# Kernel optimization log

Measured on AMD Instinct MI355X. Metric: run time of the kernel, lower is better.

The kernel has to match this reference:

```python
import jax, jax.numpy as jnp
import numpy as np

D_MODEL = 1024
NHEAD = 16
HEAD_DIM = D_MODEL // NHEAD
FF = 4096
ALPHA = 1.4142135  # deepnorm_alpha
WIN = (127, 128)   # sliding window (left, right)
EPS = 1e-5
ROPE_BASE = 10000.0


def rmsnorm(x, g):
    ms = jnp.mean(x * x, axis=-1, keepdims=True)
    return x * jax.lax.rsqrt(ms + EPS) * g


def rope(x):
    # x: [B, T, H, D]; non-interleaved rotary over full head dim
    T, D = x.shape[1], x.shape[-1]
    half = D // 2
    inv_freq = 1.0 / (ROPE_BASE ** (jnp.arange(half, dtype=jnp.float32) * 2.0 / D))
    ang = jnp.arange(T, dtype=jnp.float32)[:, None] * inv_freq[None, :]  # [T, half]
    cos = jnp.cos(ang)[None, :, None, :]
    sin = jnp.sin(ang)[None, :, None, :]
    x1, x2 = x[..., :half], x[..., half:]
    return jnp.concatenate([x1 * cos - x2 * sin, x2 * cos + x1 * sin], axis=-1)


def setup_inputs() -> dict:
    key = jax.random.key(0)
    ks = jax.random.split(key, 8)
    d, h = D_MODEL, FF
    return {
        "x": jax.random.normal(ks[0], (2, 2048, d), jnp.float32),
        "Wqkv": jax.random.normal(ks[1], (3 * d, d), jnp.float32) * 0.02,
        "Wout": jax.random.normal(ks[2], (d, d), jnp.float32) * 0.02,
        "bout": jnp.zeros((d,), jnp.float32),
        "W1": jax.random.normal(ks[3], (2 * h, d), jnp.float32) * 0.02,
        "W2": jax.random.normal(ks[4], (d, h), jnp.float32) * 0.02,
        "g1": jnp.ones((d,), jnp.float32),
        "g2": jnp.ones((d,), jnp.float32),
    }


def reference(x, Wqkv, Wout, bout, W1, W2, g1, g2):
    B, T, d = x.shape
    # --- self attention with RoPE + sliding window band mask ---
    qkv = (x @ Wqkv.T).reshape(B, T, 3, NHEAD, HEAD_DIM)
    q, k, v = qkv[:, :, 0], qkv[:, :, 1], qkv[:, :, 2]  # [B,T,H,Dh]
    q = rope(q)
    k = rope(k)
    q = jnp.swapaxes(q, 1, 2)  # [B,H,T,Dh]
    k = jnp.swapaxes(k, 1, 2)
    v = jnp.swapaxes(v, 1, 2)
    scale = 1.0 / np.sqrt(HEAD_DIM)
    scores = jnp.einsum('bhqd,bhkd->bhqk', q, k) * scale
    idx = jnp.arange(T)
    rel = idx[None, :] - idx[:, None]  # j - i
    band = (rel >= -WIN[0]) & (rel <= WIN[1])  # [T,T] allowed positions
    scores = jnp.where(band[None, None], scores, -jnp.inf)
    attn = jax.nn.softmax(scores, axis=-1)
    o = jnp.einsum('bhqk,bhkd->bhqd', attn, v)
    o = jnp.swapaxes(o, 1, 2).reshape(B, T, d)
    a = o @ Wout.T + bout
    # --- deepnorm residual 1 + RMSNorm ---
    x1 = a + ALPHA * x
    x2 = rmsnorm(x1, g1)
    # --- SwiGLU MLP: y, gate = fc1(x).chunk(2); y*gate*sigmoid(gate) ---
    yg = x2 @ W1.T
    y, gate = jnp.split(yg, 2, axis=-1)
    y = y * gate * jax.nn.sigmoid(gate)
    y = y @ W2.T
    # --- deepnorm residual 2 + RMSNorm ---
    x3 = y + ALPHA * x2
    return rmsnorm(x3, g2)
```

## Files before the change

### kernel.cpp

```cpp
#include <hip/hip_runtime.h>

#define T_SEQ   2048
#define NHEADS  16
#define DHEAD   64
#define DMODEL  1024
#define ALPHA_C 1.4142135f
#define EPS_C   1e-5f

typedef __attribute__((ext_vector_type(8))) short bf16x8;
typedef __attribute__((ext_vector_type(4))) short bf16x4;
typedef __attribute__((ext_vector_type(4))) float floatx4;

__device__ __forceinline__ float bf2f(unsigned short u) {
  union { unsigned int i; float f; } v;
  v.i = ((unsigned int)u) << 16;
  return v.f;
}
__device__ __forceinline__ unsigned short f2bf(float f) {
  union { float f; unsigned int i; } v;
  v.f = f;
  unsigned int u = v.i;
  u += 0x7FFF + ((u >> 16) & 1);
  return (unsigned short)(u >> 16);
}

__device__ __forceinline__ void gload_lds16(const void* g, void* l) {
  __builtin_amdgcn_global_load_lds(
      (const __attribute__((address_space(1))) void*)g,
      (__attribute__((address_space(3))) void*)l, 16, 0, 0);
}

__global__ void convert_all(const float* __restrict__ Wqkv,
                            const float* __restrict__ Wout,
                            const float* __restrict__ W1,
                            const float* __restrict__ W2,
                            const float* __restrict__ x,
                            unsigned short* __restrict__ ws,
                            float* __restrict__ cosT,
                            float* __restrict__ sinT)
{
  if (blockIdx.x >= 10240) {
    int gid = (blockIdx.x - 10240) * 256 + threadIdx.x;
    int t = gid >> 5, i = gid & 31;
    float fr = powf(10000.f, -(float)i * (1.f / 32.f));
    float sn, cs;
    sincosf((float)t * fr, &sn, &cs);
    cosT[gid] = cs;
    sinT[gid] = sn;
    return;
  }
  size_t i = ((size_t)blockIdx.x * 256 + threadIdx.x) * 8;
  const float* src;
  size_t off;
  if      (i <  3145728) { src = Wqkv; off = i; }
  else if (i <  4194304) { src = Wout; off = i -  3145728; }
  else if (i < 12582912) { src = W1;   off = i -  4194304; }
  else if (i < 16777216) { src = W2;   off = i - 12582912; }
  else                   { src = x;    off = i - 16777216; }
  floatx4 a = *(const floatx4*)(src + off);
  floatx4 b = *(const floatx4*)(src + off + 4);
  bf16x8 o;
  #pragma unroll
  for (int u = 0; u < 4; u++) {
    o[u]     = (short)f2bf(a[u]);
    o[4 + u] = (short)f2bf(b[u]);
  }
  *(bf16x8*)(ws + i) = o;
}

template<int BN>
__global__ __launch_bounds__(256) void gemm_lds(
    const unsigned short* __restrict__ A,
    const unsigned short* __restrict__ W,
    unsigned short* __restrict__ C,
    const float* __restrict__ bias,
    int M, int N, int K, int lda)
{
  constexpr int WN = BN / 2;
  constexpr int NJ = WN / 16;
  __shared__ unsigned short As[128 * 32];
  __shared__ unsigned short Bs[BN * 32];

  const int tid  = threadIdx.x;
  const int lane = tid & 63;
  const int wave = tid >> 6;
  const int wm = (wave >> 1) * 64;
  const int wn = (wave & 1) * WN;
  const int mBase = blockIdx.y * 128;
  const int nBase = blockIdx.x * BN;

  const int sRow = lane >> 2;
  const int sCol = (lane & 3) * 8;

  floatx4 acc[4][NJ];
  #pragma unroll
  for (int i = 0; i < 4; i++)
    #pragma unroll
    for (int j = 0; j < NJ; j++) acc[i][j] = (floatx4){0.f, 0.f, 0.f, 0.f};

  const int mrow = lane & 15;
  const int kq   = (lane >> 4) * 8;

  for (int kb = 0; kb < K; kb += 32) {
    __syncthreads();
    #pragma unroll
    for (int j = 0; j < 2; j++) {
      int r = wave * 32 + j * 16 + sRow;
      gload_lds16(A + (size_t)(mBase + r) * lda + kb + sCol,
                  &As[wave * 1024 + j * 512 + lane * 8]);
    }
    if constexpr (BN == 128) {
      #pragma unroll
      for (int j = 0; j < 2; j++) {
        int r = wave * 32 + j * 16 + sRow;
        gload_lds16(W + (size_t)(nBase + r) * K + kb + sCol,
                    &Bs[wave * 1024 + j * 512 + lane * 8]);
      }
    } else {
      int r = wave * 16 + sRow;
      gload_lds16(W + (size_t)(nBase + r) * K + kb + sCol,
                  &Bs[wave * 512 + lane * 8]);
    }
    __syncthreads();

    bf16x8 af[4], bfr[NJ];
    #pragma unroll
    for (int i = 0; i < 4; i++)
      af[i] = *(const bf16x8*)&As[(wm + i * 16 + mrow) * 32 + kq];
    #pragma unroll
    for (int j = 0; j < NJ; j++)
      bfr[j] = *(const bf16x8*)&Bs[(wn + j * 16 + mrow) * 32 + kq];
    #pragma unroll
    for (int i = 0; i < 4; i++)
      #pragma unroll
      for (int j = 0; j < NJ; j++)
        acc[i][j] = __builtin_amdgcn_mfma_f32_16x16x32_bf16(af[i], bfr[j], acc[i][j], 0, 0, 0);
  }

  const int col0 = lane & 15;
  const int row0 = (lane >> 4) * 4;
  #pragma unroll
  for (int j = 0; j < NJ; j++) {
    const int col = nBase + wn + j * 16 + col0;
    const float badd = bias ? bias[col] : 0.f;
    #pragma unroll
    for (int i = 0; i < 4; i++) {
      #pragma unroll
      for (int r = 0; r < 4; r++) {
        const int row = mBase + wm + i * 16 + row0 + r;
        C[(size_t)row * N + col] = f2bf(acc[i][j][r] + badd);
      }
    }
  }
}

#define BAR() __builtin_amdgcn_s_barrier()
#define SCB() __builtin_amdgcn_sched_barrier(0)

#define RD_A_S(bb, mh, s)                                                 \
  _Pragma("unroll") for (int i = 0; i < 4; i++)                           \
    af[i][s] = *(const bf16x8*)&lds[(bb) + aRd +                          \
        ((mh) * 64 + i * 16 + mrow) * 64 + (kq0 ^ ((s) << 5))];

#define RD_B_S(bb, s)                                                     \
  _Pragma("unroll") for (int n = 0; n < 4; n++)                           \
    bfr[n][s] = *(const bf16x8*)&lds[(bb) + bRd +                         \
        (bRow0 + n * 16 + mrow) * 64 + (kq0 ^ ((s) << 5))];

#define MFMA8(mh, nh, s)                                                  \
  _Pragma("unroll") for (int i = 0; i < 4; i++)                           \
  _Pragma("unroll") for (int n = 0; n < 2; n++)                           \
    acc[(mh) * 4 + i][(nh) * 2 + n] =                                     \
        __builtin_amdgcn_mfma_f32_16x16x32_bf16(                          \
            af[i][s], bfr[(nh) * 2 + n][s],                               \
            acc[(mh) * 4 + i][(nh) * 2 + n], 0, 0, 0);

#define KLOOP_S4()                                                        \
  for (int t = 0; t < 16; ++t) {                                          \
    const int cur = t & 1;                                                \
    const int nxt = cur ^ 1;                                              \
    const int bb  = cur * 32768;                                          \
    const int ta  = (t + 1 < 16) ? t + 1 : 15;                            \
    const int tb  = (t + 2 < 16) ? t + 2 : 15;                            \
                                                             \
    BAR();                                                                \
    stA(nxt, 1, ta);                                                      \
    RD_A_S(bb, 0, 0); RD_B_S(bb, 0);                                      \
    SCB();                                                                \
    RD_A_S(bb, 0, 1); RD_B_S(bb, 1);                                      \
    asm volatile("s_waitcnt lgkmcnt(8)" ::: "memory");                    \
    SCB();                                                                \
    __builtin_amdgcn_s_setprio(1);                                        \
    MFMA8(0, 0, 0);                                                       \
    __builtin_amdgcn_s_setprio(0);                                        \
    asm volatile("s_waitcnt lgkmcnt(0)" ::: "memory");                    \
    SCB();                                                                \
    __builtin_amdgcn_s_setprio(1);                                        \
    MFMA8(0, 0, 1);                                                       \
    __builtin_amdgcn_s_setprio(0);                                        \
                                                             \
    BAR();                                                                \
    stB(nxt, 1, ta);                                                      \
    __builtin_amdgcn_s_setprio(1);                                        \
    MFMA8(0, 1, 0); MFMA8(0, 1, 1);                                       \
    __builtin_amdgcn_s_setprio(0);                                        \
                                                             \
    BAR();                                                                \
    stB(cur, 0, tb);                                                      \
    RD_A_S(bb, 1, 0);                                                     \
    SCB();                                                                \
    RD_A_S(bb, 1, 1);                                                     \
    asm volatile("s_waitcnt lgkmcnt(4)" ::: "memory");                    \
    SCB();                                                                \
    __builtin_amdgcn_s_setprio(1);                                        \
    MFMA8(1, 1, 0);                                                       \
    __builtin_amdgcn_s_setprio(0);                                        \
    asm volatile("s_waitcnt lgkmcnt(0)" ::: "memory");                    \
    SCB();                                                                \
    __builtin_amdgcn_s_setprio(1);                                        \
    MFMA8(1, 1, 1);                                                       \
    __builtin_amdgcn_s_setprio(0);                                        \
                                                             \
    BAR();                                                                \
    stA(cur, 0, tb);                                                      \
    __builtin_amdgcn_s_setprio(1);                                        \
    MFMA8(1, 0, 0); MFMA8(1, 0, 1);                                       \
    __builtin_amdgcn_s_setprio(0);                                        \
    asm volatile("s_waitcnt vmcnt(4)" ::: "memory");                      \
  }

__global__ __launch_bounds__(512, 2) void gemm_w1_swiglu_s4(
    const unsigned short* __restrict__ A,
    const unsigned short* __restrict__ W1,
    unsigned short* __restrict__ ys)
{
  __shared__ unsigned short lds[65536];

  const int tid  = threadIdx.x;
  const int lane = tid & 63;
  const int wid  = tid >> 6;
  const int wr   = wid >> 2;
  const int wc   = wid & 3;
  const int mrow = lane & 15;
  const int quad = lane >> 4;
  const int kq0  = (quad ^ (mrow & 7)) * 8;

  const int bid  = blockIdx.x;
  const int c8   = bid & 7;
  const int u    = bid >> 3;
  const int mBase = ((c8 >> 2) * 8 + (u >> 3)) * 256;
  const int nBase = ((c8 &  3) * 8 + (u &  7)) * 128;

  const int r0 = tid >> 3;
  const int ce = (((tid & 7) ^ (r0 & 7)) * 8);
  const size_t aoff0 = (size_t)(mBase + r0) * 1024 + ce;
  const size_t aoff1 = aoff0 + (size_t)64 * 1024;
  auto growf = [&](int br) {
    int col = nBase + (br >> 6) * 32 + (br & 31);
    return ((br >> 5) & 1) ? 4096 + col : col;
  };
  const size_t boff00 = (size_t)growf(r0)       * 1024 + ce;
  const size_t boff01 = (size_t)growf(64 + r0)  * 1024 + ce;
  const size_t boff10 = (size_t)growf(128 + r0) * 1024 + ce;
  const size_t boff11 = (size_t)growf(192 + r0) * 1024 + ce;
  const int d0 = tid * 8;

  auto stA = [&](int buf, int h, int kt) {
    const unsigned short* g = A + (size_t)kt * 64 + (h ? (size_t)128 * 1024 : 0);
    int base = buf * 32768 + h * 8192;
    gload_lds16(g + aoff0, &lds[base + d0]);
    gload_lds16(g + aoff1, &lds[base + 4096 + d0]);
  };
  auto stB = [&](int buf, int h, int kt) {
    const unsigned short* g = W1 + (size_t)kt * 64;
    int base = buf * 32768 + 16384 + h * 8192;
    gload_lds16(g + (h ? boff10 : boff00), &lds[base + d0]);
    gload_lds16(g + (h ? boff11 : boff01), &lds[base + 4096 + d0]);
  };

  floatx4 acc[8][4];
  #pragma unroll
  for (int i = 0; i < 8; i++)
    #pragma unroll
    for (int n = 0; n < 4; n++) acc[i][n] = (floatx4){0.f, 0.f, 0.f, 0.f};
  bf16x8 af[4][2], bfr[4][2];

  const int aRd   = wr * 8192;
  const int bRd   = 16384 + (wc >> 1) * 8192;
  const int bRow0 = (wc & 1) * 64;

  stB(0, 0, 0); stA(0, 0, 0); stA(0, 1, 0); stB(0, 1, 0);
  stB(1, 0, 1); stA(1, 0, 1);
  asm volatile("s_waitcnt vmcnt(4)" ::: "memory");

  KLOOP_S4();

  const int col0 = lane & 15;
  const int row0 = (lane >> 4) * 4;
  #pragma unroll
  for (int n = 0; n < 2; n++) {
    const int col = nBase + wc * 32 + n * 16 + col0;
    #pragma unroll
    for (int i = 0; i < 8; i++) {
      const int rowb = mBase + wr * 128 + i * 16 + row0;
      #pragma unroll
      for (int r = 0; r < 4; r++) {
        float y = acc[i][n][r], g = acc[i][n + 2][r];
        float sig = 1.f / (1.f + __expf(-g));
        ys[(size_t)(rowb + r) * 4096 + col] = f2bf(y * g * sig);
      }
    }
  }
  asm volatile("s_waitcnt vmcnt(0)" ::: "memory");
}

__global__ __launch_bounds__(512, 2) void gemm_qkv_rope256(
    const unsigned short* __restrict__ A,
    const unsigned short* __restrict__ W,
    const float* __restrict__ cosT,
    const float* __restrict__ sinT,
    unsigned short* __restrict__ Qd,
    unsigned short* __restrict__ Kd,
    unsigned short* __restrict__ Vd)
{
  __shared__ unsigned short lds[65536];

  const int tid  = threadIdx.x;
  const int lane = tid & 63;
  const int wid  = tid >> 6;
  const int wr   = wid >> 2;
  const int wc   = wid & 3;
  const int mrow = lane & 15;
  const int quad = lane >> 4;
  const int kq0  = (quad ^ (mrow & 7)) * 8;

  const int bid  = blockIdx.x;
  const int c8   = bid & 7;
  const int u    = bid >> 3;
  const int mBase = ((c8 >> 1) * 4 + u / 6) * 256;
  const int nBase = ((c8 & 1) * 6 + u % 6) * 256;

  const int r0 = tid >> 3;
  const int ce = (((tid & 7) ^ (r0 & 7)) * 8);
  const size_t aoff0 = (size_t)(mBase + r0) * 1024 + ce;
  const size_t aoff1 = aoff0 + (size_t)64 * 1024;
  const size_t boff00 = (size_t)(nBase + r0)       * 1024 + ce;
  const size_t boff01 = (size_t)(nBase + 64 + r0)  * 1024 + ce;
  const size_t boff10 = (size_t)(nBase + 128 + r0) * 1024 + ce;
  const size_t boff11 = (size_t)(nBase + 192 + r0) * 1024 + ce;
  const int d0 = tid * 8;

  auto stA = [&](int buf, int h, int kt) {
    const unsigned short* g = A + (size_t)kt * 64 + (h ? (size_t)128 * 1024 : 0);
    int base = buf * 32768 + h * 8192;
    gload_lds16(g + aoff0, &lds[base + d0]);
    gload_lds16(g + aoff1, &lds[base + 4096 + d0]);
  };
  auto stB = [&](int buf, int h, int kt) {
    const unsigned short* g = W + (size_t)kt * 64;
    int base = buf * 32768 + 16384 + h * 8192;
    gload_lds16(g + (h ? boff10 : boff00), &lds[base + d0]);
    gload_lds16(g + (h ? boff11 : boff01), &lds[base + 4096 + d0]);
  };

  floatx4 acc[8][4];
  #pragma unroll
  for (int i = 0; i < 8; i++)
    #pragma unroll
    for (int n = 0; n < 4; n++) acc[i][n] = (floatx4){0.f, 0.f, 0.f, 0.f};
  bf16x8 af[4][2], bfr[4][2];

  const int aRd   = wr * 8192;
  const int bRd   = 16384 + (wc >> 1) * 8192;
  const int bRow0 = (wc & 1) * 64;

  stB(0, 0, 0); stA(0, 0, 0); stA(0, 1, 0); stB(0, 1, 0);
  stB(1, 0, 1); stA(1, 0, 1);
  asm volatile("s_waitcnt vmcnt(4)" ::: "memory");

  KLOOP_S4();

  const int col0 = lane & 15;
  const int row0 = (lane >> 4) * 4;
  const int colBase = nBase + wc * 64;
  const int sect = colBase >> 10;
  const int h    = (colBase & 1023) >> 6;
  unsigned short* dst = (sect == 0) ? Qd : (sect == 1) ? Kd : Vd;

  if (sect < 2) {
    #pragma unroll
    for (int i = 0; i < 8; i++) {
      #pragma unroll
      for (int r = 0; r < 4; r++) {
        const int row = mBase + wr * 128 + i * 16 + row0 + r;
        const int b = row >> 11, t = row & 2047;
        size_t ob = ((size_t)((b * NHEADS + h) * T_SEQ + t)) * DHEAD;
        const int tb = t * 32;
        float c0 = cosT[tb + col0],      s0 = sinT[tb + col0];
        float c1 = cosT[tb + col0 + 16], s1 = sinT[tb + col0 + 16];
        float x1a = acc[i][0][r], x2a = acc[i][2][r];
        float x1b = acc[i][1][r], x2b = acc[i][3][r];
        dst[ob + col0]      = f2bf(x1a * c0 - x2a * s0);
        dst[ob + col0 + 32] = f2bf(x2a * c0 + x1a * s0);
        dst[ob + col0 + 16] = f2bf(x1b * c1 - x2b * s1);
        dst[ob + col0 + 48] = f2bf(x2b * c1 + x1b * s1);
      }
    }
  } else {
    #pragma unroll
    for (int i = 0; i < 8; i++)
      #pragma unroll
      for (int n = 0; n < 4; n++)
        #pragma unroll
        for (int r = 0; r < 4; r++) {
          const int row = mBase + wr * 128 + i * 16 + row0 + r;
          const int b = row >> 11, t = row & 2047;
          dst[((size_t)((b * NHEADS + h) * T_SEQ + t)) * DHEAD + n * 16 + col0] =
              f2bf(acc[i][n][r]);
        }
  }
  asm volatile("s_waitcnt vmcnt(0)" ::: "memory");
}

#define W2_RD_A(bb, mh, s)                                                \
  _Pragma("unroll") for (int i = 0; i < 2; i++)                           \
    af[i][s] = *(const bf16x8*)&lds[(bb) +                                \
        (wr * 64 + (mh) * 32 + i * 16 + mrow) * 64 + (kq0 ^ ((s) << 5))];

#define W2_RD_B(bb, s)                                                    \
  _Pragma("unroll") for (int n = 0; n < 4; n++)                           \
    bfr[n][s] = *(const bf16x8*)&lds[(bb) + 16384 +                       \
        (wc * 64 + n * 16 + mrow) * 64 + (kq0 ^ ((s) << 5))];

#define W2_MFMA(mh, s)                                                    \
  _Pragma("unroll") for (int i = 0; i < 2; i++)                           \
  _Pragma("unroll") for (int n = 0; n < 4; n++)                           \
    acc[(mh) * 2 + i][n] =                                                \
        __builtin_amdgcn_mfma_f32_16x16x32_bf16(                          \
            af[i][s], bfr[n][s], acc[(mh) * 2 + i][n], 0, 0, 0);

__global__ __launch_bounds__(512, 2) void gemm_w2_2ph(
    const unsigned short* __restrict__ A,
    const unsigned short* __restrict__ W,
    float* __restrict__ Cp)
{
  __shared__ unsigned short lds[49152];

  const int tid  = threadIdx.x;
  const int lane = tid & 63;
  const int wid  = tid >> 6;
  const int wr   = wid >> 1;
  const int wc   = wid & 1;
  const int mrow = lane & 15;
  const int quad = lane >> 4;
  const int kq0  = (quad ^ (mrow & 7)) * 8;

  const int u  = blockIdx.x;
  const int c8 = u & 7;
  const int v  = u >> 3;
  const int zP = v >> 4;
  const int mBase = (((c8 >> 1) & 3) * 4 + ((v >> 2) & 3)) * 256;
  const int nBase = ((c8 & 1) * 4 + (v & 3)) * 128;
  const int kOff  = zP * 2048;

  const int r0 = tid >> 3;
  const int ce = (((tid & 7) ^ (r0 & 7)) * 8);
  const int d0 = tid * 8;

  auto stA = [&](int buf, int h, int kt) {
    const unsigned short* g =
        A + (size_t)(mBase + h * 128 + r0) * 4096 + kOff + kt * 64 + ce;
    int base = buf * 24576 + h * 8192;
    gload_lds16(g, &lds[base + d0]);
    gload_lds16(g + (size_t)64 * 4096, &lds[base + 4096 + d0]);
  };
  auto stB = [&](int buf, int kt) {
    const unsigned short* g =
        W + (size_t)(nBase + r0) * 4096 + kOff + kt * 64 + ce;
    int base = buf * 24576 + 16384;
    gload_lds16(g, &lds[base + d0]);
    gload_lds16(g + (size_t)64 * 4096, &lds[base + 4096 + d0]);
  };

  floatx4 acc[4][4];
  #pragma unroll
  for (int i = 0; i < 4; i++)
    #pragma unroll
    for (int n = 0; n < 4; n++) acc[i][n] = (floatx4){0.f, 0.f, 0.f, 0.f};
  bf16x8 af[2][2], bfr[4][2];

  stB(0, 0);
  stA(0, 0, 0); stA(0, 1, 0);
  stB(1, 1);
  asm volatile("s_waitcnt vmcnt(2)" ::: "memory");

  for (int t = 0; t < 32; ++t) {
    const int cur = t & 1;
    const int nxt = cur ^ 1;
    const int bb  = cur * 24576;
    const int ta  = (t + 1 < 32) ? t + 1 : 31;
    const int tb  = (t + 2 < 32) ? t + 2 : 31;

    BAR();
    stA(nxt, 0, ta); stA(nxt, 1, ta);
    W2_RD_A(bb, 0, 0); W2_RD_B(bb, 0);
    SCB();
    W2_RD_A(bb, 0, 1); W2_RD_B(bb, 1);
    asm volatile("s_waitcnt lgkmcnt(6)" ::: "memory");
    SCB();
    __builtin_amdgcn_s_setprio(1);
    W2_MFMA(0, 0);
    __builtin_amdgcn_s_setprio(0);
    asm volatile("s_waitcnt lgkmcnt(0)" ::: "memory");
    SCB();
    __builtin_amdgcn_s_setprio(1);
    W2_MFMA(0, 1);
    __builtin_amdgcn_s_setprio(0);

    BAR();
    stB(cur, tb);
    W2_RD_A(bb, 1, 0);
    SCB();
    W2_RD_A(bb, 1, 1);
    asm volatile("s_waitcnt lgkmcnt(2)" ::: "memory");
    SCB();
    __builtin_amdgcn_s_setprio(1);
    W2_MFMA(1, 0);
    __builtin_amdgcn_s_setprio(0);
    asm volatile("s_waitcnt lgkmcnt(0)" ::: "memory");
    SCB();
    __builtin_amdgcn_s_setprio(1);
    W2_MFMA(1, 1);
    __builtin_amdgcn_s_setprio(0);
    asm volatile("s_waitcnt vmcnt(2)" ::: "memory");
  }

  const int col0 = lane & 15;
  const int row0 = (lane >> 4) * 4;
  float* dst = Cp + (size_t)zP * 4096 * 1024;
  #pragma unroll
  for (int n = 0; n < 4; n++) {
    const int col = nBase + wc * 64 + n * 16 + col0;
    #pragma unroll
    for (int i = 0; i < 4; i++) {
      const int rowb = mBase + wr * 64 + i * 16 + row0;
      #pragma unroll
      for (int r = 0; r < 4; r++)
        dst[(size_t)(rowb + r) * 1024 + col] = acc[i][n][r];
    }
  }
  asm volatile("s_waitcnt vmcnt(0)" ::: "memory");
}

__global__ __launch_bounds__(256) void attn_mfma(
    const unsigned short* __restrict__ Qg,
    const unsigned short* __restrict__ Kg,
    const unsigned short* __restrict__ Vg,
    unsigned short* __restrict__ Og)
{
  __shared__ unsigned short KV[23040];
  __shared__ unsigned short Qs[64 * 72];
  __shared__ unsigned short Ps[4 * 16 * 328];

  const int tid  = threadIdx.x;
  const int lane = tid & 63;
  const int wave = tid >> 6;
  const int c    = lane & 15;
  const int quad = lane >> 4;
  const int blk  = blockIdx.x;
  const int bh   = blk >> 5;
  const int qBase = (blk & 31) * 64;
  const size_t hbase = (size_t)bh * T_SEQ * DHEAD;

  for (int e = tid; e < 320 * 8; e += 256) {
    int row = e >> 3, ch = e & 7;
    int kg = qBase - 127 + row;
    int kgc = min(max(kg, 0), T_SEQ - 1);
    *(bf16x8*)&KV[row * 72 + ch * 8] =
        *(const bf16x8*)(Kg + hbase + (size_t)kgc * DHEAD + ch * 8);
  }
  for (int e = tid; e < 64 * 8; e += 256) {
    int row = e >> 3, ch = e & 7;
    *(bf16x8*)&Qs[row * 72 + ch * 8] =
        *(const bf16x8*)(Qg + hbase + (size_t)(qBase + row) * DHEAD + ch * 8);
  }
  __syncthreads();

  bf16x8 aq[2];
  #pragma unroll
  for (int hh = 0; hh < 2; hh++)
    aq[hh] = *(const bf16x8*)&Qs[(wave * 16 + c) * 72 + hh * 32 + quad * 8];

  floatx4 s[20];
  #pragma unroll
  for (int kt = 0; kt < 20; kt++) {
    bf16x8 b0 = *(const bf16x8*)&KV[(kt * 16 + c) * 72 + quad * 8];
    bf16x8 b1 = *(const bf16x8*)&KV[(kt * 16 + c) * 72 + 32 + quad * 8];
    floatx4 t = (floatx4){0.f, 0.f, 0.f, 0.f};
    t = __builtin_amdgcn_mfma_f32_16x16x32_bf16(aq[0], b0, t, 0, 0, 0);
    t = __builtin_amdgcn_mfma_f32_16x16x32_bf16(aq[1], b1, t, 0, 0, 0);
    s[kt] = t;
  }
  __syncthreads();

  for (int ch = wave; ch < 5; ch += 4) {
    int koff = ch * 64 + lane;
    int kg = qBase - 127 + koff;
    int kgc = min(max(kg, 0), T_SEQ - 1);
    const unsigned short* vrow = Vg + hbase + (size_t)kgc * DHEAD;
    #pragma unroll
    for (int dg = 0; dg < 8; dg++) {
      bf16x8 v8 = *(const bf16x8*)(vrow + dg * 8);
      #pragma unroll
      for (int j = 0; j < 8; j++)
        KV[(dg * 8 + j) * 328 + koff] = (unsigned short)v8[j];
    }
  }

  const int kLoMin = max(0, 127 - qBase);
  const int kHiMax = min(319, 2047 + 127 - qBase);
  float mx[4] = {-3e38f, -3e38f, -3e38f, -3e38f};
  #pragma unroll
  for (int kt = 0; kt < 20; kt++) {
    const int koff = kt * 16 + c;
    #pragma unroll
    for (int reg = 0; reg < 4; reg++) {
      const int qrow = wave * 16 + quad * 4 + reg;
      const int d = koff - qrow;
      bool ok = (d >= 0) && (d <= 255) && (koff >= kLoMin) && (koff <= kHiMax);
      float val = ok ? s[kt][reg] * 0.125f : -3e38f;
      s[kt][reg] = val;
      mx[reg] = fmaxf(mx[reg], val);
    }
  }
  #pragma unroll
  for (int reg = 0; reg < 4; reg++)
    #pragma unroll
    for (int m = 1; m <= 8; m <<= 1)
      mx[reg] = fmaxf(mx[reg], __shfl_xor(mx[reg], m));

  float ls[4] = {0.f, 0.f, 0.f, 0.f};
  #pragma unroll
  for (int kt = 0; kt < 20; kt++) {
    const int koff = kt * 16 + c;
    #pragma unroll
    for (int reg = 0; reg < 4; reg++) {
      float p = __expf(s[kt][reg] - mx[reg]);
      ls[reg] += p;
      Ps[wave * 5248 + (quad * 4 + reg) * 328 + koff] = f2bf(p);
    }
  }
  float inv[4];
  #pragma unroll
  for (int reg = 0; reg < 4; reg++) {
    #pragma unroll
    for (int m = 1; m <= 8; m <<= 1) ls[reg] += __shfl_xor(ls[reg], m);
    inv[reg] = 1.f / ls[reg];
  }
  __syncthreads();

  floatx4 oacc[4];
  #pragma unroll
  for (int nt = 0; nt < 4; nt++) oacc[nt] = (floatx4){0.f, 0.f, 0.f, 0.f};
  #pragma unroll
  for (int kt2 = 0; kt2 < 10; kt2++) {
    bf16x8 a = *(const bf16x8*)&Ps[wave * 5248 + c * 328 + kt2 * 32 + quad * 8];
    #pragma unroll
    for (int nt = 0; nt < 4; nt++) {
      bf16x8 bb = *(const bf16x8*)&KV[(nt * 16 + c) * 328 + kt2 * 32 + quad * 8];
      oacc[nt] = __builtin_amdgcn_mfma_f32_16x16x32_bf16(a, bb, oacc[nt], 0, 0, 0);
    }
  }

  const int b = bh >> 4, h = bh & 15;
  #pragma unroll
  for (int nt = 0; nt < 4; nt++) {
    #pragma unroll
    for (int reg = 0; reg < 4; reg++) {
      const int qg = qBase + wave * 16 + quad * 4 + reg;
      Og[((size_t)(b * T_SEQ + qg)) * DMODEL + h * DHEAD + nt * 16 + c] =
          f2bf(oacc[nt][reg] * inv[reg]);
    }
  }
}

__global__ __launch_bounds__(256) void rmsnorm_mid(
    const unsigned short* __restrict__ a,
    const float* __restrict__ x,
    const float* __restrict__ g,
    unsigned short* __restrict__ out)
{
  __shared__ float red[4];
  const int row = blockIdx.x;
  const int tid = threadIdx.x;
  const size_t base = (size_t)row * DMODEL;
  const int c = tid * 4;
  bf16x4  av = *(const bf16x4*)(a + base + c);
  floatx4 xv = *(const floatx4*)(x + base + c);
  floatx4 gv = *(const floatx4*)(g + c);
  float s[4], ss = 0.f;
  #pragma unroll
  for (int j = 0; j < 4; j++) {
    s[j] = bf2f((unsigned short)av[j]) + ALPHA_C * xv[j];
    ss += s[j] * s[j];
  }
  #pragma unroll
  for (int m = 1; m <= 32; m <<= 1) ss += __shfl_xor(ss, m);
  if ((tid & 63) == 0) red[tid >> 6] = ss;
  __syncthreads();
  float ms = (red[0] + red[1] + red[2] + red[3]) * (1.f / DMODEL);
  float scl = rsqrtf(ms + EPS_C);
  bf16x4 ov;
  #pragma unroll
  for (int j = 0; j < 4; j++) ov[j] = (short)f2bf(s[j] * scl * gv[j]);
  *(bf16x4*)(out + base + c) = ov;
}

__global__ __launch_bounds__(256) void rmsnorm_final_sk(
    const float* __restrict__ p0,
    const float* __restrict__ p1,
    const unsigned short* __restrict__ x2,
    const float* __restrict__ g,
    float* __restrict__ out)
{
  __shared__ float red[4];
  const int row = blockIdx.x;
  const int tid = threadIdx.x;
  const size_t base = (size_t)row * DMODEL;
  const int c = tid * 4;
  floatx4 a0 = *(const floatx4*)(p0 + base + c);
  floatx4 a1 = *(const floatx4*)(p1 + base + c);
  bf16x4  xv = *(const bf16x4*)(x2 + base + c);
  floatx4 gv = *(const floatx4*)(g + c);
  float s[4], ss = 0.f;
  #pragma unroll
  for (int j = 0; j < 4; j++) {
    s[j] = (a0[j] + a1[j]) + ALPHA_C * bf2f((unsigned short)xv[j]);
    ss += s[j] * s[j];
  }
  #pragma unroll
  for (int m = 1; m <= 32; m <<= 1) ss += __shfl_xor(ss, m);
  if ((tid & 63) == 0) red[tid >> 6] = ss;
  __syncthreads();
  float ms = (red[0] + red[1] + red[2] + red[3]) * (1.f / DMODEL);
  float scl = rsqrtf(ms + EPS_C);
  floatx4 ov;
  #pragma unroll
  for (int j = 0; j < 4; j++) ov[j] = s[j] * scl * gv[j];
  *(floatx4*)(out + base + c) = ov;
}

extern "C" void kernel_launch(void* const* d_in, const int* in_sizes, int n_in,
                              void* d_out, int out_size, void* d_ws, size_t ws_size,
                              hipStream_t stream) {
  (void)in_sizes; (void)n_in; (void)out_size; (void)ws_size;
  const float* x    = (const float*)d_in[0];
  const float* Wqkv = (const float*)d_in[1];
  const float* Wout = (const float*)d_in[2];
  const float* bout = (const float*)d_in[3];
  const float* W1   = (const float*)d_in[4];
  const float* W2   = (const float*)d_in[5];
  const float* g1   = (const float*)d_in[6];
  const float* g2   = (const float*)d_in[7];
  float* out = (float*)d_out;

  unsigned short* ws    = (unsigned short*)d_ws;
  unsigned short* Wqkvb = ws;
  unsigned short* Woutb = ws + 3145728;
  unsigned short* W1b   = ws + 4194304;
  unsigned short* W2b   = ws + 12582912;
  unsigned short* P1    = ws + 16777216;
  unsigned short* x2    = ws + 20971520;
  unsigned short* q     = ws + 25165824;
  unsigned short* k     = ws + 29360128;
  unsigned short* v     = ws + 33554432;
  unsigned short* o     = ws + 37748736;
  unsigned short* ys    = ws + 25165824;
  float* cosT = (float*)(ws + 37748736);
  float* sinT = cosT + 65536;
  float* p0   = (float*)(ws + 41943040);

  convert_all<<<10496, 256, 0, stream>>>(Wqkv, Wout, W1, W2, x, ws, cosT, sinT);
  gemm_qkv_rope256<<<192, 512, 0, stream>>>(P1, Wqkvb, cosT, sinT, q, k, v);
  attn_mfma<<<32 * (T_SEQ / 64), 256, 0, stream>>>(q, k, v, o);
  gemm_lds<64><<<dim3(16, 32), 256, 0, stream>>>(o, Woutb, P1, bout, 4096, 1024, 1024, 1024);
  rmsnorm_mid<<<4096, 256, 0, stream>>>(P1, x, g1, x2);
  gemm_w1_swiglu_s4<<<512, 512, 0, stream>>>(x2, W1b, ys);
  gemm_w2_2ph<<<256, 512, 0, stream>>>(ys, W2b, p0);
  rmsnorm_final_sk<<<4096, 256, 0, stream>>>(p0, p0 + 4194304, x2, g2, out);
}
```

Measured before the change: 350.0 us.

## Replace simple Wout GEMM with double-buffered swizzled two-phase MFMA kernel

Swaps the basic LDS GEMM for the output projection (4096x1024x1024) for a new kernel that reuses the W2 GEMM's software-pipelined k-loop. It has 256x128 tiles, XOR-swizzled LDS, double buffering, sched barriers and priority hints. The W2 loop body is factored into a macro so both kernels share it. The aim is to overlap global loads with MFMA work and raise compute efficiency. The trade-off is only 128 blocks on a GPU with many CUs, so occupancy and tail effects may limit the gain.

```diff
diff --git a/kernel.cpp b/kernel.cpp
--- a/kernel.cpp
+++ b/kernel.cpp
@@ -68,92 +68,6 @@
   *(bf16x8*)(ws + i) = o;
 }
 
-template<int BN>
-__global__ __launch_bounds__(256) void gemm_lds(
-    const unsigned short* __restrict__ A,
-    const unsigned short* __restrict__ W,
-    unsigned short* __restrict__ C,
-    const float* __restrict__ bias,
-    int M, int N, int K, int lda)
-{
-  constexpr int WN = BN / 2;
-  constexpr int NJ = WN / 16;
-  __shared__ unsigned short As[128 * 32];
-  __shared__ unsigned short Bs[BN * 32];
-
-  const int tid  = threadIdx.x;
-  const int lane = tid & 63;
-  const int wave = tid >> 6;
-  const int wm = (wave >> 1) * 64;
-  const int wn = (wave & 1) * WN;
-  const int mBase = blockIdx.y * 128;
-  const int nBase = blockIdx.x * BN;
-
-  const int sRow = lane >> 2;
-  const int sCol = (lane & 3) * 8;
-
-  floatx4 acc[4][NJ];
-  #pragma unroll
-  for (int i = 0; i < 4; i++)
-    #pragma unroll
-    for (int j = 0; j < NJ; j++) acc[i][j] = (floatx4){0.f, 0.f, 0.f, 0.f};
-
-  const int mrow = lane & 15;
-  const int kq   = (lane >> 4) * 8;
-
-  for (int kb = 0; kb < K; kb += 32) {
-    __syncthreads();
-    #pragma unroll
-    for (int j = 0; j < 2; j++) {
-      int r = wave * 32 + j * 16 + sRow;
-      gload_lds16(A + (size_t)(mBase + r) * lda + kb + sCol,
-                  &As[wave * 1024 + j * 512 + lane * 8]);
-    }
-    if constexpr (BN == 128) {
-      #pragma unroll
-      for (int j = 0; j < 2; j++) {
-        int r = wave * 32 + j * 16 + sRow;
-        gload_lds16(W + (size_t)(nBase + r) * K + kb + sCol,
-                    &Bs[wave * 1024 + j * 512 + lane * 8]);
-      }
-    } else {
-      int r = wave * 16 + sRow;
-      gload_lds16(W + (size_t)(nBase + r) * K + kb + sCol,
-                  &Bs[wave * 512 + lane * 8]);
-    }
-    __syncthreads();
-
-    bf16x8 af[4], bfr[NJ];
-    #pragma unroll
-    for (int i = 0; i < 4; i++)
-      af[i] = *(const bf16x8*)&As[(wm + i * 16 + mrow) * 32 + kq];
-    #pragma unroll
-    for (int j = 0; j < NJ; j++)
-      bfr[j] = *(const bf16x8*)&Bs[(wn + j * 16 + mrow) * 32 + kq];
-    #pragma unroll
-    for (int i = 0; i < 4; i++)
-      #pragma unroll
-      for (int j = 0; j < NJ; j++)
-        acc[i][j] = __builtin_amdgcn_mfma_f32_16x16x32_bf16(af[i], bfr[j], acc[i][j], 0, 0, 0);
-  }
-
-  const int col0 = lane & 15;
-  const int row0 = (lane >> 4) * 4;
-  #pragma unroll
-  for (int j = 0; j < NJ; j++) {
-    const int col = nBase + wn + j * 16 + col0;
-    const float badd = bias ? bias[col] : 0.f;
-    #pragma unroll
-    for (int i = 0; i < 4; i++) {
-      #pragma unroll
-      for (int r = 0; r < 4; r++) {
-        const int row = mBase + wm + i * 16 + row0 + r;
-        C[(size_t)row * N + col] = f2bf(acc[i][j][r] + badd);
-      }
-    }
-  }
-}
-
 #define BAR() __builtin_amdgcn_s_barrier()
 #define SCB() __builtin_amdgcn_sched_barrier(0)
 
@@ -439,6 +353,46 @@
         __builtin_amdgcn_mfma_f32_16x16x32_bf16(                          \
             af[i][s], bfr[n][s], acc[(mh) * 2 + i][n], 0, 0, 0);
 
+#define W2_KLOOP(NT)                                                      \
+  for (int t = 0; t < (NT); ++t) {                                        \
+    const int cur = t & 1;                                                \
+    const int nxt = cur ^ 1;                                              \
+    const int bb  = cur * 24576;                                          \
+    const int ta  = (t + 1 < (NT)) ? t + 1 : (NT) - 1;                    \
+    const int tb  = (t + 2 < (NT)) ? t + 2 : (NT) - 1;                    \
+    BAR();                                                                \
+    stA(nxt, 0, ta); stA(nxt, 1, ta);                                     \
+    W2_RD_A(bb, 0, 0); W2_RD_B(bb, 0);                                    \
+    SCB();                                                                \
+    W2_RD_A(bb, 0, 1); W2_RD_B(bb, 1);                                    \
+    asm volatile("s_waitcnt lgkmcnt(6)" ::: "memory");                    \
+    SCB();                                                                \
+    __builtin_amdgcn_s_setprio(1);                                        \
+    W2_MFMA(0, 0);                                                        \
+    __builtin_amdgcn_s_setprio(0);                                        \
+    asm volatile("s_waitcnt lgkmcnt(0)" ::: "memory");                    \
+    SCB();                                                                \
+    __builtin_amdgcn_s_setprio(1);                                        \
+    W2_MFMA(0, 1);                                                        \
+    __builtin_amdgcn_s_setprio(0);                                        \
+    BAR();                                                                \
+    stB(cur, tb);                                                         \
+    W2_RD_A(bb, 1, 0);                                                    \
+    SCB();                                                                \
+    W2_RD_A(bb, 1, 1);                                                    \
+    asm volatile("s_waitcnt lgkmcnt(2)" ::: "memory");                    \
+    SCB();                                                                \
+    __builtin_amdgcn_s_setprio(1);                                        \
+    W2_MFMA(1, 0);                                                        \
+    __builtin_amdgcn_s_setprio(0);                                        \
+    asm volatile("s_waitcnt lgkmcnt(0)" ::: "memory");                    \
+    SCB();                                                                \
+    __builtin_amdgcn_s_setprio(1);                                        \
+    W2_MFMA(1, 1);                                                        \
+    __builtin_amdgcn_s_setprio(0);                                        \
+    asm volatile("s_waitcnt vmcnt(2)" ::: "memory");                      \
+  }
+
 __global__ __launch_bounds__(512, 2) void gemm_w2_2ph(
     const unsigned short* __restrict__ A,
     const unsigned short* __restrict__ W,
@@ -494,46 +448,7 @@
   stB(1, 1);
   asm volatile("s_waitcnt vmcnt(2)" ::: "memory");
 
-  for (int t = 0; t < 32; ++t) {
-    const int cur = t & 1;
-    const int nxt = cur ^ 1;
-    const int bb  = cur * 24576;
-    const int ta  = (t + 1 < 32) ? t + 1 : 31;
-    const int tb  = (t + 2 < 32) ? t + 2 : 31;
-
-    BAR();
-    stA(nxt, 0, ta); stA(nxt, 1, ta);
-    W2_RD_A(bb, 0, 0); W2_RD_B(bb, 0);
-    SCB();
-    W2_RD_A(bb, 0, 1); W2_RD_B(bb, 1);
-    asm volatile("s_waitcnt lgkmcnt(6)" ::: "memory");
-    SCB();
-    __builtin_amdgcn_s_setprio(1);
-    W2_MFMA(0, 0);
-    __builtin_amdgcn_s_setprio(0);
-    asm volatile("s_waitcnt lgkmcnt(0)" ::: "memory");
-    SCB();
-    __builtin_amdgcn_s_setprio(1);
-    W2_MFMA(0, 1);
-    __builtin_amdgcn_s_setprio(0);
-
-    BAR();
-    stB(cur, tb);
-    W2_RD_A(bb, 1, 0);
-    SCB();
-    W2_RD_A(bb, 1, 1);
-    asm volatile("s_waitcnt lgkmcnt(2)" ::: "memory");
-    SCB();
-    __builtin_amdgcn_s_setprio(1);
-    W2_MFMA(1, 0);
-    __builtin_amdgcn_s_setprio(0);
-    asm volatile("s_waitcnt lgkmcnt(0)" ::: "memory");
-    SCB();
-    __builtin_amdgcn_s_setprio(1);
-    W2_MFMA(1, 1);
-    __builtin_amdgcn_s_setprio(0);
-    asm volatile("s_waitcnt vmcnt(2)" ::: "memory");
-  }
+  W2_KLOOP(32);
 
   const int col0 = lane & 15;
   const int row0 = (lane >> 4) * 4;
@@ -547,6 +462,79 @@
       #pragma unroll
       for (int r = 0; r < 4; r++)
         dst[(size_t)(rowb + r) * 1024 + col] = acc[i][n][r];
+    }
+  }
+  asm volatile("s_waitcnt vmcnt(0)" ::: "memory");
+}
+
+__global__ __launch_bounds__(512, 2) void gemm_wout_2ph(
+    const unsigned short* __restrict__ A,
+    const unsigned short* __restrict__ W,
+    const float* __restrict__ bias,
+    unsigned short* __restrict__ C)
+{
+  __shared__ unsigned short lds[49152];
+
+  const int tid  = threadIdx.x;
+  const int lane = tid & 63;
+  const int wid  = tid >> 6;
+  const int wr   = wid >> 1;
+  const int wc   = wid & 1;
+  const int mrow = lane & 15;
+  const int quad = lane >> 4;
+  const int kq0  = (quad ^ (mrow & 7)) * 8;
+
+  const int u  = blockIdx.x;
+  const int c8 = u & 7;
+  const int v  = u >> 3;
+  const int mBase = ((c8 >> 1) * 4 + (v >> 2)) * 256;
+  const int nBase = ((c8 & 1) * 4 + (v & 3)) * 128;
+
+  const int r0 = tid >> 3;
+  const int ce = (((tid & 7) ^ (r0 & 7)) * 8);
+  const int d0 = tid * 8;
+
+  auto stA = [&](int buf, int h, int kt) {
+    const unsigned short* g =
+        A + (size_t)(mBase + h * 128 + r0) * 1024 + kt * 64 + ce;
+    int base = buf * 24576 + h * 8192;
+    gload_lds16(g, &lds[base + d0]);
+    gload_lds16(g + (size_t)64 * 1024, &lds[base + 4096 + d0]);
+  };
+  auto stB = [&](int buf, int kt) {
+    const unsigned short* g =
+        W + (size_t)(nBase + r0) * 1024 + kt * 64 + ce;
+    int base = buf * 24576 + 16384;
+    gload_lds16(g, &lds[base + d0]);
+    gload_lds16(g + (size_t)64 * 1024, &lds[base + 4096 + d0]);
+  };
+
+  floatx4 acc[4][4];
+  #pragma unroll
+  for (int i = 0; i < 4; i++)
+    #pragma unroll
+    for (int n = 0; n < 4; n++) acc[i][n] = (floatx4){0.f, 0.f, 0.f, 0.f};
+  bf16x8 af[2][2], bfr[4][2];
+
+  stB(0, 0);
+  stA(0, 0, 0); stA(0, 1, 0);
+  stB(1, 1);
+  asm volatile("s_waitcnt vmcnt(2)" ::: "memory");
+
+  W2_KLOOP(16);
+
+  const int col0 = lane & 15;
+  const int row0 = (lane >> 4) * 4;
+  #pragma unroll
+  for (int n = 0; n < 4; n++) {
+    const int col = nBase + wc * 64 + n * 16 + col0;
+    const float badd = bias[col];
+    #pragma unroll
+    for (int i = 0; i < 4; i++) {
+      const int rowb = mBase + wr * 64 + i * 16 + row0;
+      #pragma unroll
+      for (int r = 0; r < 4; r++)
+        C[(size_t)(rowb + r) * 1024 + col] = f2bf(acc[i][n][r] + badd);
     }
   }
   asm volatile("s_waitcnt vmcnt(0)" ::: "memory");
@@ -783,7 +771,7 @@
   convert_all<<<10496, 256, 0, stream>>>(Wqkv, Wout, W1, W2, x, ws, cosT, sinT);
   gemm_qkv_rope256<<<192, 512, 0, stream>>>(P1, Wqkvb, cosT, sinT, q, k, v);
   attn_mfma<<<32 * (T_SEQ / 64), 256, 0, stream>>>(q, k, v, o);
-  gemm_lds<64><<<dim3(16, 32), 256, 0, stream>>>(o, Woutb, P1, bout, 4096, 1024, 1024, 1024);
+  gemm_wout_2ph<<<128, 512, 0, stream>>>(o, Woutb, bout, P1);
   rmsnorm_mid<<<4096, 256, 0, stream>>>(P1, x, g1, x2);
   gemm_w1_swiglu_s4<<<512, 512, 0, stream>>>(x2, W1b, ys);
   gemm_w2_2ph<<<256, 512, 0, stream>>>(ys, W2b, p0);
```

Result: no change. 350.5 us (+0.1%).
